# Kernel tuning notes

Measured on AMD Instinct MI355X. Metric: run time of the kernel, lower is better.

The kernel has to match this reference:

```python
import jax, jax.numpy as jnp
import numpy as np

H = 1024       # hidden_size
NH = 16        # num heads
HD = H // NH   # head dim
EPS = 1e-12


def setup_inputs() -> dict:
    key = jax.random.key(0)
    ks = jax.random.split(key, 12)
    s = 1.0 / np.sqrt(H)
    return {
        "hidden_states": jax.random.normal(ks[0], (2, 2048, H), jnp.float32),
        "attention_mask": jnp.zeros((2, 1, 1, 2048), jnp.float32),
        "wq": jax.random.uniform(ks[1], (H, H), jnp.float32, -s, s),
        "bq": jnp.zeros((H,), jnp.float32),
        "wk": jax.random.uniform(ks[2], (H, H), jnp.float32, -s, s),
        "bk": jnp.zeros((H,), jnp.float32),
        "wv": jax.random.uniform(ks[3], (H, H), jnp.float32, -s, s),
        "bv": jnp.zeros((H,), jnp.float32),
        "wo": jax.random.uniform(ks[4], (H, H), jnp.float32, -s, s),
        "bo": jnp.zeros((H,), jnp.float32),
        "ln_gamma": jnp.ones((H,), jnp.float32),
        "ln_beta": jnp.zeros((H,), jnp.float32),
    }


def reference(hidden_states, attention_mask, wq, bq, wk, bk, wv, bv, wo, bo, ln_gamma, ln_beta):
    residual = hidden_states
    # pre-LayerNorm
    mu = jnp.mean(hidden_states, axis=-1, keepdims=True)
    var = jnp.var(hidden_states, axis=-1, keepdims=True)
    x = (hidden_states - mu) / jnp.sqrt(var + EPS) * ln_gamma + ln_beta

    B, S, _ = x.shape
    # QKV projections (torch Linear: x @ W.T + b), split heads -> [B, NH, S, HD]
    def proj(w, b):
        return (x @ w.T + b).reshape(B, S, NH, HD).transpose(0, 2, 1, 3)
    q = proj(wq, bq)
    k = proj(wk, bk)
    v = proj(wv, bv)

    scores = jnp.einsum("bhqd,bhkd->bhqk", q, k) / np.sqrt(HD).astype(np.float32)
    scores = scores + attention_mask  # broadcast additive mask
    probs = jax.nn.softmax(scores, axis=-1)
    ctx = jnp.einsum("bhqk,bhkd->bhqd", probs, v)
    ctx = ctx.transpose(0, 2, 1, 3).reshape(B, S, NH * HD)

    out = ctx @ wo.T + bo
    return out + residual
```

## Files before the change

kernel.cpp:

```cpp
#include <hip/hip_runtime.h>
#include <cstdint>

typedef unsigned short u16;
typedef __bf16  bf16x8 __attribute__((ext_vector_type(8)));
typedef unsigned short u16x8 __attribute__((ext_vector_type(8)));
typedef unsigned short u16x4 __attribute__((ext_vector_type(4)));
typedef float   f32x4  __attribute__((ext_vector_type(4)));

#define LOG2E 1.44269504088896340736f

__device__ __forceinline__ u16 f2b(float f) {
  union { __bf16 h; u16 u; } c; c.h = (__bf16)f;
  return c.u;
}

__device__ __forceinline__ int swz(int row) { return (row & 7) ^ ((row >> 3) & 7); }
__device__ __forceinline__ int sidx(int row, int k) {
  return row * 64 + ((((k >> 3) ^ swz(row)) & 7) << 3) + (k & 7);
}
__device__ __forceinline__ bf16x8 ld_frag(const u16* base, int row, int k) {
  return *(const bf16x8*)(base + sidx(row, k));
}

__device__ __forceinline__ void async16(const u16* g, u16* l) {
  __builtin_amdgcn_global_load_lds(
      (__attribute__((address_space(1))) unsigned int*)(uintptr_t)g,
      (__attribute__((address_space(3))) unsigned int*)(uintptr_t)l,
      16, 0, 0);
}

__global__ __launch_bounds__(256) void prep_kernel(
    const float* __restrict__ hs, const float* __restrict__ gamma,
    const float* __restrict__ beta, u16* __restrict__ X,
    const float* __restrict__ w0, const float* __restrict__ w1,
    const float* __restrict__ w2, const float* __restrict__ w3,
    u16* __restrict__ Wd) {
  const int tid = threadIdx.x;
  if (blockIdx.x >= 4096) {
    const int idx4 = blockIdx.x - 4096;
    const int mat = idx4 >> 10;
    const float* src = (mat == 0) ? w0 : (mat == 1) ? w1 : (mat == 2) ? w2 : w3;
    const int idx = ((idx4 & 1023) * 256 + tid) * 4;
    f32x4 v = *(const f32x4*)(src + idx);
    u16x4 o;
#pragma unroll
    for (int j = 0; j < 4; ++j) o[j] = f2b(v[j]);
    *(u16x4*)(Wd + (size_t)mat * 1048576 + idx) = o;
    return;
  }
  __shared__ float red[8];
  const int row = blockIdx.x;
  f32x4 v = *(const f32x4*)(hs + (size_t)row * 1024 + tid * 4);
  float s = 0.f, s2 = 0.f;
#pragma unroll
  for (int j = 0; j < 4; ++j) { s += v[j]; s2 += v[j] * v[j]; }
#pragma unroll
  for (int o = 1; o < 64; o <<= 1) { s += __shfl_xor(s, o); s2 += __shfl_xor(s2, o); }
  const int wid = tid >> 6, lane = tid & 63;
  if (lane == 0) { red[wid] = s; red[4 + wid] = s2; }
  __syncthreads();
  s  = red[0] + red[1] + red[2] + red[3];
  s2 = red[4] + red[5] + red[6] + red[7];
  const float mean = s * (1.f / 1024.f);
  const float var  = fmaxf(s2 * (1.f / 1024.f) - mean * mean, 0.f);
  const float rstd = rsqrtf(var + 1e-12f);
  f32x4 g = *(const f32x4*)(gamma + tid * 4);
  f32x4 bb = *(const f32x4*)(beta + tid * 4);
  u16x4 outv;
#pragma unroll
  for (int j = 0; j < 4; ++j) outv[j] = f2b((v[j] - mean) * rstd * g[j] + bb[j]);
  *(u16x4*)(X + (size_t)row * 1024 + tid * 4) = outv;
}

template <int MODE>
__device__ __forceinline__ void gemm_tile_128(
    const u16* __restrict__ A, const u16* __restrict__ Bt,
    const float* __restrict__ bias, const float* __restrict__ res,
    void* __restrict__ Cv, int ldc, int m0, int nG) {
  __shared__ __align__(16) u16 As[128 * 64];
  __shared__ __align__(16) u16 Bs[128 * 64];
  const int tid = threadIdx.x;
  const int wid = tid >> 6;
  const int lane = tid & 63;
  const int l15 = lane & 15, lq = lane >> 4;
  const int wm = (wid & 1) << 6, wn = (wid >> 1) << 6;
  const int srow = tid >> 3;
  const int sg = tid & 7;

  f32x4 acc[4][4] = {};
  u16x8 ar[4], br[4];

#pragma unroll
  for (int i = 0; i < 4; ++i) {
    int row = (i << 5) + srow;
    ar[i] = *(const u16x8*)(A  + (size_t)row * 1024 + (sg << 3));
    br[i] = *(const u16x8*)(Bt + (size_t)row * 1024 + (sg << 3));
  }

  for (int k0 = 0; k0 < 1024; k0 += 64) {
    if (k0) __syncthreads();
#pragma unroll
    for (int i = 0; i < 4; ++i) {
      int row = (i << 5) + srow;
      *(u16x8*)(As + sidx(row, sg << 3)) = ar[i];
      *(u16x8*)(Bs + sidx(row, sg << 3)) = br[i];
    }
    __syncthreads();
    if (k0 + 64 < 1024) {
#pragma unroll
      for (int i = 0; i < 4; ++i) {
        int row = (i << 5) + srow;
        ar[i] = *(const u16x8*)(A  + (size_t)row * 1024 + k0 + 64 + (sg << 3));
        br[i] = *(const u16x8*)(Bt + (size_t)row * 1024 + k0 + 64 + (sg << 3));
      }
    }
#pragma unroll
    for (int kk = 0; kk < 2; ++kk) {
      bf16x8 af[4], bf[4];
#pragma unroll
      for (int mi = 0; mi < 4; ++mi) af[mi] = ld_frag(As, wm + (mi << 4) + l15, (kk << 5) + (lq << 3));
#pragma unroll
      for (int ni = 0; ni < 4; ++ni) bf[ni] = ld_frag(Bs, wn + (ni << 4) + l15, (kk << 5) + (lq << 3));
#pragma unroll
      for (int mi = 0; mi < 4; ++mi)
#pragma unroll
        for (int ni = 0; ni < 4; ++ni)
          acc[mi][ni] = __builtin_amdgcn_mfma_f32_16x16x32_bf16(af[mi], bf[ni], acc[mi][ni], 0, 0, 0);
    }
  }
  __syncthreads();

  if (MODE == 2) {
    u16* Rg = (wid < 2 ? As : Bs) + ((wid & 1) << 12);
#pragma unroll
    for (int ni = 0; ni < 4; ++ni) {
      const float bv = bias[wn + (ni << 4) + l15];
#pragma unroll
      for (int mi = 0; mi < 4; ++mi) {
        u16x4 pk;
#pragma unroll
        for (int r = 0; r < 4; ++r) pk[r] = f2b(acc[mi][ni][r] + bv);
        *(u16x4*)(Rg + sidx((ni << 4) + l15, (mi << 4) + (lq << 2))) = pk;
      }
    }
    __asm__ volatile("" ::: "memory");
    const int rrow = lane >> 3;
    const int rg8  = (lane & 7) << 3;
    const int mg0 = m0 + wm;
    const int bb = mg0 >> 11, ss0 = mg0 & 2047;
    const int hh = (nG + wn) >> 6;
    u16* vbase = (u16*)Cv + ((size_t)((bb << 4) + hh) * 64) * 2048 + ss0;
#pragma unroll
    for (int p = 0; p < 8; ++p) {
      const int nl = (p << 3) + rrow;
      bf16x8 rowv = ld_frag(Rg, nl, rg8);
      *(bf16x8*)(vbase + (size_t)nl * 2048 + rg8) = rowv;
    }
  } else {
#pragma unroll
    for (int ni = 0; ni < 4; ++ni) {
      const int n = wn + (ni << 4) + l15;
      const float bv = bias[n];
#pragma unroll
      for (int mi = 0; mi < 4; ++mi) {
#pragma unroll
        for (int r = 0; r < 4; ++r) {
          const int m = wm + (mi << 4) + (lq << 2) + r;
          float v = acc[mi][ni][r] + bv;
          if (MODE == 1) {
            v += res[(size_t)m * ldc + n];
            ((float*)Cv)[(size_t)m * ldc + n] = v;
          } else {
            ((u16*)Cv)[(size_t)m * ldc + n] = f2b(v);
          }
        }
      }
    }
  }
}

__global__ __launch_bounds__(256, 3) void qkv_kernel(
    const u16* __restrict__ X, const u16* __restrict__ W,
    const float* __restrict__ bq, const float* __restrict__ bk, const float* __restrict__ bv,
    u16* __restrict__ QK, u16* __restrict__ VT) {
  const int n0 = blockIdx.x << 7;
  const int m0 = blockIdx.y << 7;
  const int wsel = n0 >> 10;
  const int nloc = n0 & 1023;
  const u16* Bt = W + (size_t)wsel * 1048576 + (size_t)nloc * 1024;
  if (wsel < 2) {
    const float* bias = (wsel == 0 ? bq : bk) + nloc;
    gemm_tile_128<0>(X + (size_t)m0 * 1024, Bt, bias, nullptr,
                     QK + (size_t)m0 * 2048 + n0, 2048, 0, 0);
  } else {
    gemm_tile_128<2>(X + (size_t)m0 * 1024, Bt, bv + nloc, nullptr,
                     VT, 0, m0, nloc);
  }
}

__global__ __launch_bounds__(256, 3) void out_kernel(
    const u16* __restrict__ CTX, const u16* __restrict__ wo,
    const float* __restrict__ bo, const float* __restrict__ res, float* __restrict__ OUT) {
  const int n0 = blockIdx.x << 7;
  const int m0 = blockIdx.y << 7;
  gemm_tile_128<1>(CTX + (size_t)m0 * 1024, wo + (size_t)n0 * 1024, bo + n0,
                   res + (size_t)m0 * 1024 + n0, OUT + (size_t)m0 * 1024 + n0, 1024, 0, 0);
}

__global__ __launch_bounds__(256, 2) void attn_kernel(
    const u16* __restrict__ QK, const u16* __restrict__ VT,
    const float* __restrict__ mask, u16* __restrict__ CTX) {
  __shared__ __align__(16) u16 Ksb[2][64 * 64];
  __shared__ __align__(16) u16 Vtsb[2][64 * 64];
  __shared__ __align__(16) u16 Ps[4 * 32 * 64];
  const int tid = threadIdx.x;
  const int wid = tid >> 6;
  const int lane = tid & 63;
  const int l15 = lane & 15, lq = lane >> 4;
  const int qt = blockIdx.x, h = blockIdx.y, b = blockIdx.z;

  const int qbase = (b << 11) + (qt << 7) + (wid << 5);
  const u16* Kbase  = QK + (size_t)(b << 11) * 2048 + 1024 + (h << 6);
  const u16* VTbase = VT + (size_t)(((b << 4) + h) << 6) * 2048;

  bf16x8 qf[2][2];
#pragma unroll
  for (int f = 0; f < 2; ++f)
#pragma unroll
    for (int kc = 0; kc < 2; ++kc)
      qf[f][kc] = *(const bf16x8*)(QK + (size_t)(qbase + (f << 4) + l15) * 2048 + (h << 6) + (kc << 5) + (lq << 3));

  f32x4 cacc[2][4] = {};
  float l_run[2] = {0.f, 0.f};

  const int sg = lane & 7;
  const int srow0 = (wid << 4) + (lane >> 3);
  const int srow1 = srow0 + 8;
  const int gk0 = ((sg ^ swz(srow0)) & 7) << 3;
  const int gk1 = ((sg ^ swz(srow1)) & 7) << 3;
  const int ld0 = ((wid << 1) + 0) << 9;
  const int ld1 = ((wid << 1) + 1) << 9;
  u16* Pw = Ps + (wid << 11);

  async16(Kbase + (size_t)srow0 * 2048 + gk0, &Ksb[0][0] + ld0);
  async16(Kbase + (size_t)srow1 * 2048 + gk1, &Ksb[0][0] + ld1);
  async16(VTbase + (size_t)srow0 * 2048 + gk0, &Vtsb[0][0] + ld0);
  async16(VTbase + (size_t)srow1 * 2048 + gk1, &Vtsb[0][0] + ld1);

  for (int kt = 0; kt < 32; ++kt) {
    const u16* Ks  = &Ksb[kt & 1][0];
    const u16* Vts = &Vtsb[kt & 1][0];
    __syncthreads();
    if (kt + 1 < 32) {
      const int nk = (kt + 1) << 6;
      async16(Kbase + (size_t)(nk + srow0) * 2048 + gk0, &Ksb[(kt + 1) & 1][0] + ld0);
      async16(Kbase + (size_t)(nk + srow1) * 2048 + gk1, &Ksb[(kt + 1) & 1][0] + ld1);
      async16(VTbase + (size_t)srow0 * 2048 + nk + gk0, &Vtsb[(kt + 1) & 1][0] + ld0);
      async16(VTbase + (size_t)srow1 * 2048 + nk + gk1, &Vtsb[(kt + 1) & 1][0] + ld1);
    }

    f32x4 sacc[2][4] = {};
#pragma unroll
    for (int kc = 0; kc < 2; ++kc) {
      bf16x8 kf[4];
#pragma unroll
      for (int ki = 0; ki < 4; ++ki) kf[ki] = ld_frag(Ks, (ki << 4) + l15, (kc << 5) + (lq << 3));
#pragma unroll
      for (int f = 0; f < 2; ++f)
#pragma unroll
        for (int ki = 0; ki < 4; ++ki)
          sacc[f][ki] = __builtin_amdgcn_mfma_f32_16x16x32_bf16(kf[ki], qf[f][kc], sacc[f][ki], 0, 0, 0);
    }

    f32x4 mvl[4];
#pragma unroll
    for (int ki = 0; ki < 4; ++ki) {
      f32x4 mv = *(const f32x4*)(mask + (b << 11) + (kt << 6) + (ki << 4) + (lq << 2));
#pragma unroll
      for (int r = 0; r < 4; ++r) mvl[ki][r] = mv[r] * LOG2E;
    }

#pragma unroll
    for (int f = 0; f < 2; ++f) {
      float rs = 0.f;
#pragma unroll
      for (int ki = 0; ki < 4; ++ki) {
#pragma unroll
        for (int r = 0; r < 4; ++r) {
          float pv = __builtin_amdgcn_exp2f(sacc[f][ki][r] * (0.125f * LOG2E) + mvl[ki][r]);
          sacc[f][ki][r] = pv;
          rs += pv;
        }
      }
      l_run[f] += rs;
#pragma unroll
      for (int ki = 0; ki < 4; ++ki) {
        u16x4 pk;
#pragma unroll
        for (int r = 0; r < 4; ++r) pk[r] = f2b(sacc[f][ki][r]);
        *(u16x4*)(Pw + sidx((f << 4) + l15, (ki << 4) + (lq << 2))) = pk;
      }
    }
    __asm__ volatile("" ::: "memory");

#pragma unroll
    for (int kc = 0; kc < 2; ++kc) {
      bf16x8 pf[2];
#pragma unroll
      for (int f = 0; f < 2; ++f) pf[f] = ld_frag(Pw, (f << 4) + l15, (kc << 5) + (lq << 3));
#pragma unroll
      for (int dm = 0; dm < 4; ++dm) {
        bf16x8 vf = ld_frag(Vts, (dm << 4) + l15, (kc << 5) + (lq << 3));
#pragma unroll
        for (int f = 0; f < 2; ++f)
          cacc[f][dm] = __builtin_amdgcn_mfma_f32_16x16x32_bf16(vf, pf[f], cacc[f][dm], 0, 0, 0);
      }
    }
  }

#pragma unroll
  for (int f = 0; f < 2; ++f) {
    float rs = l_run[f];
    rs += __shfl_xor(rs, 16);
    rs += __shfl_xor(rs, 32);
    const float inv = 1.0f / rs;
    u16* Crow = CTX + (size_t)(qbase + (f << 4) + l15) * 1024 + (h << 6);
#pragma unroll
    for (int dm = 0; dm < 4; ++dm) {
      u16x4 o;
#pragma unroll
      for (int r = 0; r < 4; ++r) o[r] = f2b(cacc[f][dm][r] * inv);
      *(u16x4*)(Crow + (dm << 4) + (lq << 2)) = o;
    }
  }
}

extern "C" void kernel_launch(void* const* d_in, const int* in_sizes, int n_in,
                              void* d_out, int out_size, void* d_ws, size_t ws_size,
                              hipStream_t stream) {
  const float* hs   = (const float*)d_in[0];
  const float* mask = (const float*)d_in[1];
  const float* wq   = (const float*)d_in[2];
  const float* bq   = (const float*)d_in[3];
  const float* wk   = (const float*)d_in[4];
  const float* bk   = (const float*)d_in[5];
  const float* wv   = (const float*)d_in[6];
  const float* bv   = (const float*)d_in[7];
  const float* wo   = (const float*)d_in[8];
  const float* bo   = (const float*)d_in[9];
  const float* lg   = (const float*)d_in[10];
  const float* lb   = (const float*)d_in[11];

  u16* X   = (u16*)d_ws;
  u16* QK  = X + (size_t)4096 * 1024;
  u16* CTX = QK + (size_t)4096 * 2048;
  u16* W   = CTX + (size_t)4096 * 1024;
  u16* VT  = W + (size_t)4 * 1048576;
  float* OUT = (float*)d_out;

  prep_kernel<<<8192, 256, 0, stream>>>(hs, lg, lb, X, wq, wk, wv, wo, W);
  qkv_kernel<<<dim3(24, 32), 256, 0, stream>>>(X, W, bq, bk, bv, QK, VT);
  attn_kernel<<<dim3(16, 16, 2), 256, 0, stream>>>(QK, VT, mask, CTX);
  out_kernel<<<dim3(8, 32), 256, 0, stream>>>(CTX, W + (size_t)3 * 1048576, bo, hs, OUT);
}
```

Baseline: 211.8 us.

## Use 32x32x16 MFMA in attention with register-resident P via permlane swap

Rewrites the attention inner loop to use 32x32x16 bf16 MFMAs instead of 16x16x32. The probabilities are packed with v_cvt_pk_bf16_f32 and rearranged into B-operand layout with permlane32_swap, which removes the per-wave LDS staging buffer and its write/read round trip. It also flattens the grid to 1D with a swizzled block-to-(q-tile, head, batch) mapping, likely to improve K/V cache locality. The fragment layout math is intricate, and the register pressure from the f32x16 accumulators could limit occupancy.

```diff
diff --git a/kernel.cpp b/kernel.cpp
--- a/kernel.cpp
+++ b/kernel.cpp
@@ -6,6 +6,7 @@
 typedef unsigned short u16x8 __attribute__((ext_vector_type(8)));
 typedef unsigned short u16x4 __attribute__((ext_vector_type(4)));
 typedef float   f32x4  __attribute__((ext_vector_type(4)));
+typedef float   f32x16 __attribute__((ext_vector_type(16)));
 
 #define LOG2E 1.44269504088896340736f
 
@@ -27,6 +28,11 @@
       (__attribute__((address_space(1))) unsigned int*)(uintptr_t)g,
       (__attribute__((address_space(3))) unsigned int*)(uintptr_t)l,
       16, 0, 0);
+}
+
+__device__ __forceinline__ void plswap(unsigned int &a, unsigned int &b) {
+  auto r = __builtin_amdgcn_permlane32_swap(a, b, false, false);
+  a = r[0]; b = r[1];
 }
 
 __global__ __launch_bounds__(256) void prep_kernel(
@@ -212,40 +218,44 @@
     const float* __restrict__ mask, u16* __restrict__ CTX) {
   __shared__ __align__(16) u16 Ksb[2][64 * 64];
   __shared__ __align__(16) u16 Vtsb[2][64 * 64];
-  __shared__ __align__(16) u16 Ps[4 * 32 * 64];
   const int tid = threadIdx.x;
   const int wid = tid >> 6;
   const int lane = tid & 63;
-  const int l15 = lane & 15, lq = lane >> 4;
-  const int qt = blockIdx.x, h = blockIdx.y, b = blockIdx.z;
+  const int l31 = lane & 31, b5 = lane >> 5;
+
+  const int lid = blockIdx.x;
+  const int sw = ((lid & 7) << 6) | (lid >> 3);
+  const int qt = sw & 15;
+  const int hz = sw >> 4;
+  const int h = hz & 15;
+  const int b = hz >> 4;
 
   const int qbase = (b << 11) + (qt << 7) + (wid << 5);
   const u16* Kbase  = QK + (size_t)(b << 11) * 2048 + 1024 + (h << 6);
   const u16* VTbase = VT + (size_t)(((b << 4) + h) << 6) * 2048;
 
-  bf16x8 qf[2][2];
-#pragma unroll
-  for (int f = 0; f < 2; ++f)
-#pragma unroll
-    for (int kc = 0; kc < 2; ++kc)
-      qf[f][kc] = *(const bf16x8*)(QK + (size_t)(qbase + (f << 4) + l15) * 2048 + (h << 6) + (kc << 5) + (lq << 3));
-
-  f32x4 cacc[2][4] = {};
-  float l_run[2] = {0.f, 0.f};
+  bf16x8 qf[4];
+#pragma unroll
+  for (int ds = 0; ds < 4; ++ds)
+    qf[ds] = *(const bf16x8*)(QK + (size_t)(qbase + l31) * 2048 + (h << 6) + (ds << 4) + (b5 << 3));
+
+  f32x16 cacc[2] = {};
+  float l_run = 0.f;
 
   const int sg = lane & 7;
   const int srow0 = (wid << 4) + (lane >> 3);
   const int srow1 = srow0 + 8;
   const int gk0 = ((sg ^ swz(srow0)) & 7) << 3;
   const int gk1 = ((sg ^ swz(srow1)) & 7) << 3;
-  const int ld0 = ((wid << 1) + 0) << 9;
-  const int ld1 = ((wid << 1) + 1) << 9;
-  u16* Pw = Ps + (wid << 11);
+  const int ld0 = (wid << 10);
+  const int ld1 = (wid << 10) + 512;
 
   async16(Kbase + (size_t)srow0 * 2048 + gk0, &Ksb[0][0] + ld0);
   async16(Kbase + (size_t)srow1 * 2048 + gk1, &Ksb[0][0] + ld1);
   async16(VTbase + (size_t)srow0 * 2048 + gk0, &Vtsb[0][0] + ld0);
   async16(VTbase + (size_t)srow1 * 2048 + gk1, &Vtsb[0][0] + ld1);
+
+  const float c1 = 0.125f * LOG2E;
 
   for (int kt = 0; kt < 32; ++kt) {
     const u16* Ks  = &Ksb[kt & 1][0];
@@ -259,80 +269,69 @@
       async16(VTbase + (size_t)srow1 * 2048 + nk + gk1, &Vtsb[(kt + 1) & 1][0] + ld1);
     }
 
-    f32x4 sacc[2][4] = {};
-#pragma unroll
-    for (int kc = 0; kc < 2; ++kc) {
-      bf16x8 kf[4];
-#pragma unroll
-      for (int ki = 0; ki < 4; ++ki) kf[ki] = ld_frag(Ks, (ki << 4) + l15, (kc << 5) + (lq << 3));
-#pragma unroll
-      for (int f = 0; f < 2; ++f)
-#pragma unroll
-        for (int ki = 0; ki < 4; ++ki)
-          sacc[f][ki] = __builtin_amdgcn_mfma_f32_16x16x32_bf16(kf[ki], qf[f][kc], sacc[f][ki], 0, 0, 0);
-    }
-
-    f32x4 mvl[4];
-#pragma unroll
-    for (int ki = 0; ki < 4; ++ki) {
-      f32x4 mv = *(const f32x4*)(mask + (b << 11) + (kt << 6) + (ki << 4) + (lq << 2));
-#pragma unroll
-      for (int r = 0; r < 4; ++r) mvl[ki][r] = mv[r] * LOG2E;
-    }
-
-#pragma unroll
-    for (int f = 0; f < 2; ++f) {
-      float rs = 0.f;
-#pragma unroll
-      for (int ki = 0; ki < 4; ++ki) {
-#pragma unroll
-        for (int r = 0; r < 4; ++r) {
-          float pv = __builtin_amdgcn_exp2f(sacc[f][ki][r] * (0.125f * LOG2E) + mvl[ki][r]);
-          sacc[f][ki][r] = pv;
-          rs += pv;
+    f32x16 sacc[2] = {};
+#pragma unroll
+    for (int ds = 0; ds < 4; ++ds) {
+      bf16x8 kf0 = ld_frag(Ks, l31,      (ds << 4) + (b5 << 3));
+      bf16x8 kf1 = ld_frag(Ks, 32 + l31, (ds << 4) + (b5 << 3));
+      sacc[0] = __builtin_amdgcn_mfma_f32_32x32x16_bf16(kf0, qf[ds], sacc[0], 0, 0, 0);
+      sacc[1] = __builtin_amdgcn_mfma_f32_32x32x16_bf16(kf1, qf[ds], sacc[1], 0, 0, 0);
+    }
+
+    unsigned int pw[2][8];
+#pragma unroll
+    for (int ki = 0; ki < 2; ++ki) {
+      float pv[16];
+#pragma unroll
+      for (int rr = 0; rr < 4; ++rr) {
+        f32x4 mv = *(const f32x4*)(mask + (b << 11) + (kt << 6) + (ki << 5) + (rr << 3) + (b5 << 2));
+#pragma unroll
+        for (int c = 0; c < 4; ++c) {
+          float p = __builtin_amdgcn_exp2f(sacc[ki][(rr << 2) + c] * c1 + mv[c] * LOG2E);
+          pv[(rr << 2) + c] = p;
+          l_run += p;
         }
       }
-      l_run[f] += rs;
-#pragma unroll
-      for (int ki = 0; ki < 4; ++ki) {
-        u16x4 pk;
-#pragma unroll
-        for (int r = 0; r < 4; ++r) pk[r] = f2b(sacc[f][ki][r]);
-        *(u16x4*)(Pw + sidx((f << 4) + l15, (ki << 4) + (lq << 2))) = pk;
-      }
-    }
-    __asm__ volatile("" ::: "memory");
-
-#pragma unroll
-    for (int kc = 0; kc < 2; ++kc) {
-      bf16x8 pf[2];
-#pragma unroll
-      for (int f = 0; f < 2; ++f) pf[f] = ld_frag(Pw, (f << 4) + l15, (kc << 5) + (lq << 3));
-#pragma unroll
-      for (int dm = 0; dm < 4; ++dm) {
-        bf16x8 vf = ld_frag(Vts, (dm << 4) + l15, (kc << 5) + (lq << 3));
-#pragma unroll
-        for (int f = 0; f < 2; ++f)
-          cacc[f][dm] = __builtin_amdgcn_mfma_f32_16x16x32_bf16(vf, pf[f], cacc[f][dm], 0, 0, 0);
-      }
-    }
-  }
-
-#pragma unroll
-  for (int f = 0; f < 2; ++f) {
-    float rs = l_run[f];
-    rs += __shfl_xor(rs, 16);
-    rs += __shfl_xor(rs, 32);
-    const float inv = 1.0f / rs;
-    u16* Crow = CTX + (size_t)(qbase + (f << 4) + l15) * 1024 + (h << 6);
-#pragma unroll
-    for (int dm = 0; dm < 4; ++dm) {
+#pragma unroll
+      for (int j = 0; j < 8; ++j) {
+        unsigned int w;
+        asm("v_cvt_pk_bf16_f32 %0, %1, %2" : "=v"(w) : "v"(pv[2 * j]), "v"(pv[2 * j + 1]));
+        pw[ki][j] = w;
+      }
+      plswap(pw[ki][0], pw[ki][2]);
+      plswap(pw[ki][1], pw[ki][3]);
+      plswap(pw[ki][4], pw[ki][6]);
+      plswap(pw[ki][5], pw[ki][7]);
+    }
+
+#pragma unroll
+    for (int ki = 0; ki < 2; ++ki)
+#pragma unroll
+      for (int kb = 0; kb < 2; ++kb) {
+        union { unsigned int u[4]; bf16x8 v; } pcvt;
+#pragma unroll
+        for (int j = 0; j < 4; ++j) pcvt.u[j] = pw[ki][(kb << 2) + j];
+        const bf16x8 pf = pcvt.v;
+#pragma unroll
+        for (int dm = 0; dm < 2; ++dm) {
+          bf16x8 vf = ld_frag(Vts, (dm << 5) + l31, (ki << 5) + (kb << 4) + (b5 << 3));
+          cacc[dm] = __builtin_amdgcn_mfma_f32_32x32x16_bf16(vf, pf, cacc[dm], 0, 0, 0);
+        }
+      }
+  }
+
+  l_run += __shfl_xor(l_run, 32);
+  const float inv = 1.0f / l_run;
+  u16* Crow = CTX + (size_t)(qbase + l31) * 1024 + (h << 6);
+#pragma unroll
+  for (int dm = 0; dm < 2; ++dm)
+#pragma unroll
+    for (int rr = 0; rr < 4; ++rr) {
       u16x4 o;
 #pragma unroll
-      for (int r = 0; r < 4; ++r) o[r] = f2b(cacc[f][dm][r] * inv);
-      *(u16x4*)(Crow + (dm << 4) + (lq << 2)) = o;
-    }
-  }
+      for (int c = 0; c < 4; ++c) o[c] = f2b(cacc[dm][(rr << 2) + c] * inv);
+      *(u16x4*)(Crow + (dm << 5) + (rr << 3) + (b5 << 2)) = o;
+    }
 }
 
 extern "C" void kernel_launch(void* const* d_in, const int* in_sizes, int n_in,
@@ -360,6 +359,6 @@
 
   prep_kernel<<<8192, 256, 0, stream>>>(hs, lg, lb, X, wq, wk, wv, wo, W);
   qkv_kernel<<<dim3(24, 32), 256, 0, stream>>>(X, W, bq, bk, bv, QK, VT);
-  attn_kernel<<<dim3(16, 16, 2), 256, 0, stream>>>(QK, VT, mask, CTX);
+  attn_kernel<<<dim3(512), 256, 0, stream>>>(QK, VT, mask, CTX);
   out_kernel<<<dim3(8, 32), 256, 0, stream>>>(CTX, W + (size_t)3 * 1048576, bo, hs, OUT);
 }
```

After: 216.6 us. 1.02x slower.
